# Kernel optimization log

Hardware: AMD Instinct MI355X
Metric: run time of the kernel (lower is better)

Reference implementation:

```python
import jax, jax.numpy as jnp
import numpy as np

B, V, D, H = 16, 20000, 256, 256
EPS = 1e-5


def _ln(x, g, b):
    m = jnp.mean(x, axis=-1, keepdims=True)
    v = jnp.mean(jnp.square(x - m), axis=-1, keepdims=True)
    return (x - m) * jax.lax.rsqrt(v + EPS) * g + b


def setup_inputs() -> dict:
    key = jax.random.key(0)
    ks = jax.random.split(key, 8)
    s = 1.0 / np.sqrt(D)
    return {
        "patient_emb": jax.random.normal(ks[0], (B, D), jnp.float32),
        "atc4_emb_matrix": jax.random.normal(ks[1], (V, D), jnp.float32),
        "Wp": jax.random.normal(ks[2], (D, D), jnp.float32) * s,
        "bp": jnp.zeros((D,), jnp.float32),
        "gp": jnp.ones((D,), jnp.float32),
        "betap": jnp.zeros((D,), jnp.float32),
        "Wa": jax.random.normal(ks[3], (D, D), jnp.float32) * s,
        "ba": jnp.zeros((D,), jnp.float32),
        "ga": jnp.ones((D,), jnp.float32),
        "betaa": jnp.zeros((D,), jnp.float32),
        "W1": jax.random.normal(ks[4], (2 * D, H), jnp.float32) * (1.0 / np.sqrt(2 * D)),
        "b1": jnp.zeros((H,), jnp.float32),
        "W2": jax.random.normal(ks[5], (H,), jnp.float32) * (1.0 / np.sqrt(H)),
        "b2": jnp.zeros((1,), jnp.float32),
        "g_pred": jnp.ones((V,), jnp.float32),
        "b_pred": jnp.zeros((V,), jnp.float32),
    }


def reference(patient_emb, atc4_emb_matrix, Wp, bp, gp, betap, Wa, ba, ga, betaa,
              W1, b1, W2, b2, g_pred, b_pred):
    # patient projector + layernorm: (B, D)
    p = _ln(patient_emb @ Wp + bp, gp, betap)
    # atc4 projector + layernorm: (V, D)
    a = _ln(atc4_emb_matrix @ Wa + ba, ga, betaa)
    # AttentionFusion: concat([p_expand, a_expand], -1) @ W1 == p@W1[:D] + a@W1[D:]
    ph = p @ W1[:D]            # (B, H)
    ah = a @ W1[D:]            # (V, H)
    h = jnp.tanh(ph[:, None, :] + ah[None, :, :] + b1)   # (B, V, H)
    scores = jnp.einsum('bvh,h->bv', h, W2) + b2[0]       # (B, V)
    # pred layernorm over the vocab dimension
    return _ln(scores, g_pred, b_pred)
```

## Files before the change

kernel.cpp:

```cpp
#include <hip/hip_runtime.h>


typedef unsigned short ushort_t;
typedef __attribute__((ext_vector_type(8))) short short8;
typedef __attribute__((ext_vector_type(4))) float floatx4;

#define C2F 2.8853900817779268f
#define V_N 20000
#define NBLK 625

__device__ __forceinline__ ushort_t f2bf(float f) {
    unsigned int u = __builtin_bit_cast(unsigned int, f);
    u += 0x7FFFu + ((u >> 16) & 1u);
    return (ushort_t)(u >> 16);
}
__device__ __forceinline__ float exp2_fast(float x) { return __builtin_amdgcn_exp2f(x); }
__device__ __forceinline__ float rcp_fast(float x)  { return __builtin_amdgcn_rcpf(x); }

__global__ __launch_bounds__(1024) void prep_kernel(
    const float* __restrict__ patient_emb, const float* __restrict__ Wp,
    const float* __restrict__ bp, const float* __restrict__ gp,
    const float* __restrict__ betap, const float* __restrict__ Wa,
    const float* __restrict__ W1, ushort_t* __restrict__ pWa,
    ushort_t* __restrict__ pW1b, float* __restrict__ EpT)
{
    const int blk = blockIdx.x;
    const int tid = threadIdx.x;
    __shared__ float peL[256];
    __shared__ float pL[256];
    __shared__ float part[4][256];
    __shared__ float red[8];

    if (blk < 16) {
        int slot = blk * 1024 + tid;
        int matrix = slot >> 13;
        int rest = slot & 8191;
        int s = rest >> 10, T = (rest >> 6) & 15, l = rest & 63;
        const float* src = matrix ? (W1 + 256 * 256) : Wa;
        ushort_t* dst = matrix ? pW1b : pWa;
        int kbase = s * 32 + ((l >> 4) << 3);
        int nn = (T << 4) + (l & 15);
        short8 t;
        #pragma unroll
        for (int j = 0; j < 8; ++j)
            t[j] = (short)f2bf(src[(kbase + j) * 256 + nn]);
        *(short8*)(dst + rest * 8) = t;
        return;
    }

    const int b = blk - 16;
    const int j = tid & 255, pq = tid >> 8;
    if (tid < 256) peL[tid] = patient_emb[b * 256 + tid];
    __syncthreads();
    float a0 = 0.f;
    #pragma unroll 8
    for (int dd = 0; dd < 64; ++dd) {
        int d = pq * 64 + dd;
        a0 += peL[d] * Wp[d * 256 + j];
    }
    part[pq][j] = a0;
    __syncthreads();
    float x = 0.f;
    if (tid < 256) {
        x = part[0][j] + part[1][j] + part[2][j] + part[3][j] + bp[j];
        float s1 = x, s2 = x * x;
        #pragma unroll
        for (int off = 32; off; off >>= 1) {
            s1 += __shfl_xor(s1, off);
            s2 += __shfl_xor(s2, off);
        }
        int wv = tid >> 6;
        if ((tid & 63) == 0) { red[wv * 2] = s1; red[wv * 2 + 1] = s2; }
    }
    __syncthreads();
    if (tid < 256) {
        float s1 = red[0] + red[2] + red[4] + red[6];
        float s2 = red[1] + red[3] + red[5] + red[7];
        float mean = s1 * (1.f / 256.f);
        float var  = s2 * (1.f / 256.f) - mean * mean;
        float rstd = rsqrtf(var + 1e-5f);
        pL[tid] = (x - mean) * rstd * gp[tid] + betap[tid];
    }
    __syncthreads();
    float a2 = 0.f;
    #pragma unroll 8
    for (int dd = 0; dd < 64; ++dd) {
        int d = pq * 64 + dd;
        a2 += pL[d] * W1[d * 256 + j];
    }
    part[pq][j] = a2;
    __syncthreads();
    if (tid < 256)
        EpT[tid * 16 + b] = exp2_fast(
            C2F * (part[0][tid] + part[1][tid] + part[2][tid] + part[3][tid]));
}

__global__ __launch_bounds__(256) void mega_kernel(
    const float* __restrict__ atc4, const float* __restrict__ ba,
    const float* __restrict__ ga, const float* __restrict__ betaa,
    const float* __restrict__ b1, const float* __restrict__ W2,
    const ushort_t* __restrict__ pWa, const ushort_t* __restrict__ pW1b,
    const float* __restrict__ EpT, float* __restrict__ scores,
    float* __restrict__ s1g, float* __restrict__ s2g)
{
    __shared__ ushort_t AtileF[8192];
    __shared__ float EpL[256 * 17];
    __shared__ float statsP[4][32][2];
    __shared__ float statsF[32][2];
    __shared__ float redbuf[2][1056];

    const int tid = threadIdx.x;
    const int w = tid >> 6, lane = tid & 63;
    const int q = lane >> 4, n = lane & 15;
    const int v0 = blockIdx.x * 32;

    #pragma unroll
    for (int i = 0; i < 16; ++i) {
        int idx = i * 256 + tid;
        EpL[(idx >> 4) * 17 + (idx & 15)] = EpT[idx];
    }
    {
        const int r_ = tid >> 3, s_ = tid & 7;
        const int mi_ = r_ >> 4, n_ = r_ & 15;
        const float* srcp = atc4 + (v0 + r_) * 256 + s_ * 32;
        #pragma unroll
        for (int j = 0; j < 8; ++j) {
            float4 f = ((const float4*)srcp)[j];
            ushort4 usv = make_ushort4(f2bf(f.x), f2bf(f.y), f2bf(f.z), f2bf(f.w));
            int addr = ((mi_ * 8 + s_) * 64 + (j >> 1) * 16 + n_) * 8 + (j & 1) * 4;
            *(ushort4*)(AtileF + addr) = usv;
        }
    }
    __syncthreads();

    floatx4 acc[2][4];
    #pragma unroll
    for (int mi = 0; mi < 2; ++mi)
        #pragma unroll
        for (int ni = 0; ni < 4; ++ni) acc[mi][ni] = (floatx4){0.f, 0.f, 0.f, 0.f};
    #pragma unroll
    for (int s = 0; s < 8; ++s) {
        short8 a0 = ((const short8*)AtileF)[s * 64 + lane];
        short8 a1 = ((const short8*)AtileF)[(8 + s) * 64 + lane];
        #pragma unroll
        for (int ni = 0; ni < 4; ++ni) {
            short8 bfv = *(const short8*)(pWa + ((s * 16 + w * 4 + ni) * 64 + lane) * 8);
            acc[0][ni] = __builtin_amdgcn_mfma_f32_16x16x32_bf16(a0, bfv, acc[0][ni], 0, 0, 0);
            acc[1][ni] = __builtin_amdgcn_mfma_f32_16x16x32_bf16(a1, bfv, acc[1][ni], 0, 0, 0);
        }
    }

    float bac[4], gac[4], bec[4], b1c[4], w2c[4];
    #pragma unroll
    for (int ni = 0; ni < 4; ++ni) {
        int col = w * 64 + ni * 16 + n;
        bac[ni] = ba[col]; gac[ni] = ga[col]; bec[ni] = betaa[col];
        b1c[ni] = C2F * b1[col]; w2c[ni] = W2[col];
    }

    float s1v[8] = {0, 0, 0, 0, 0, 0, 0, 0}, s2v[8] = {0, 0, 0, 0, 0, 0, 0, 0};
    #pragma unroll
    for (int mi = 0; mi < 2; ++mi)
        #pragma unroll
        for (int ni = 0; ni < 4; ++ni)
            #pragma unroll
            for (int r = 0; r < 4; ++r) {
                float x = acc[mi][ni][r] + bac[ni];
                acc[mi][ni][r] = x;
                s1v[mi * 4 + r] += x;
                s2v[mi * 4 + r] += x * x;
            }
    #pragma unroll
    for (int off = 1; off < 16; off <<= 1)
        #pragma unroll
        for (int k = 0; k < 8; ++k) {
            s1v[k] += __shfl_xor(s1v[k], off);
            s2v[k] += __shfl_xor(s2v[k], off);
        }
    if (n == 0) {
        #pragma unroll
        for (int mi = 0; mi < 2; ++mi)
            #pragma unroll
            for (int r = 0; r < 4; ++r) {
                int row = mi * 16 + q * 4 + r;
                statsP[w][row][0] = s1v[mi * 4 + r];
                statsP[w][row][1] = s2v[mi * 4 + r];
            }
    }
    __syncthreads();
    if (tid < 32) {
        float m1 = statsP[0][tid][0] + statsP[1][tid][0] + statsP[2][tid][0] + statsP[3][tid][0];
        float m2 = statsP[0][tid][1] + statsP[1][tid][1] + statsP[2][tid][1] + statsP[3][tid][1];
        float mean = m1 * (1.f / 256.f);
        float var  = m2 * (1.f / 256.f) - mean * mean;
        statsF[tid][0] = mean;
        statsF[tid][1] = rsqrtf(var + 1e-5f);
    }
    __syncthreads();

    #pragma unroll
    for (int mi = 0; mi < 2; ++mi)
        #pragma unroll
        for (int r = 0; r < 4; ++r) {
            int row = mi * 16 + q * 4 + r;
            float mean = statsF[row][0], rstd = statsF[row][1];
            #pragma unroll
            for (int ni = 0; ni < 4; ++ni) {
                float xv = (acc[mi][ni][r] - mean) * rstd * gac[ni] + bec[ni];
                int addr = ((mi * 8 + (w * 2 + (ni >> 1))) * 64 +
                            ((ni & 1) * 2 + (n >> 3)) * 16 + (q * 4 + r)) * 8 + (n & 7);
                AtileF[addr] = f2bf(xv);
            }
        }
    __syncthreads();

    floatx4 acc2[2][4];
    #pragma unroll
    for (int mi = 0; mi < 2; ++mi)
        #pragma unroll
        for (int ni = 0; ni < 4; ++ni) acc2[mi][ni] = (floatx4){0.f, 0.f, 0.f, 0.f};
    #pragma unroll
    for (int s = 0; s < 8; ++s) {
        short8 a0 = ((const short8*)AtileF)[s * 64 + lane];
        short8 a1 = ((const short8*)AtileF)[(8 + s) * 64 + lane];
        #pragma unroll
        for (int ni = 0; ni < 4; ++ni) {
            short8 bfv = *(const short8*)(pW1b + ((s * 16 + w * 4 + ni) * 64 + lane) * 8);
            acc2[0][ni] = __builtin_amdgcn_mfma_f32_16x16x32_bf16(a0, bfv, acc2[0][ni], 0, 0, 0);
            acc2[1][ni] = __builtin_amdgcn_mfma_f32_16x16x32_bf16(a1, bfv, acc2[1][ni], 0, 0, 0);
        }
    }

    float Ea[2][4][4];
    #pragma unroll
    for (int mi = 0; mi < 2; ++mi)
        #pragma unroll
        for (int ni = 0; ni < 4; ++ni)
            #pragma unroll
            for (int r = 0; r < 4; ++r)
                Ea[mi][ni][r] = exp2_fast(fmaf(C2F, acc2[mi][ni][r], b1c[ni]));

    #pragma unroll
    for (int p = 0; p < 2; ++p) {
        float accs[8][8];
        #pragma unroll
        for (int bb = 0; bb < 8; ++bb)
            #pragma unroll
            for (int v = 0; v < 8; ++v) accs[bb][v] = 0.f;
        #pragma unroll
        for (int ni = 0; ni < 4; ++ni) {
            int base = (w * 64 + ni * 16 + n) * 17 + p * 8;
            float ep[8];
            #pragma unroll
            for (int bb = 0; bb < 8; ++bb) ep[bb] = EpL[base + bb];
            #pragma unroll
            for (int bb = 0; bb < 8; ++bb)
                #pragma unroll
                for (int mi = 0; mi < 2; ++mi)
                    #pragma unroll
                    for (int r = 0; r < 4; ++r)
                        accs[bb][mi * 4 + r] +=
                            w2c[ni] * rcp_fast(fmaf(ep[bb], Ea[mi][ni][r], 1.f));
        }
        float t4[4][8], t2v[2][8], t1[8], afin[8];
        {
            int hb = n & 1;
            #pragma unroll
            for (int p2 = 0; p2 < 4; ++p2)
                #pragma unroll
                for (int v = 0; v < 8; ++v) {
                    float keep = hb ? accs[2 * p2 + 1][v] : accs[2 * p2][v];
                    float send = hb ? accs[2 * p2][v] : accs[2 * p2 + 1][v];
                    t4[p2][v] = keep + __shfl_xor(send, 1);
                }
            hb = (n >> 1) & 1;
            #pragma unroll
            for (int p2 = 0; p2 < 2; ++p2)
                #pragma unroll
                for (int v = 0; v < 8; ++v) {
                    float keep = hb ? t4[2 * p2 + 1][v] : t4[2 * p2][v];
                    float send = hb ? t4[2 * p2][v] : t4[2 * p2 + 1][v];
                    t2v[p2][v] = keep + __shfl_xor(send, 2);
                }
            hb = (n >> 2) & 1;
            #pragma unroll
            for (int v = 0; v < 8; ++v) {
                float keep = hb ? t2v[1][v] : t2v[0][v];
                float send = hb ? t2v[0][v] : t2v[1][v];
                t1[v] = keep + __shfl_xor(send, 4);
            }
            #pragma unroll
            for (int v = 0; v < 8; ++v)
                afin[v] = t1[v] + __shfl_xor(t1[v], 8);
        }
        if (n < 8) {
            #pragma unroll
            for (int mi = 0; mi < 2; ++mi)
                #pragma unroll
                for (int r = 0; r < 4; ++r)
                    redbuf[p][(w * 8 + n) * 33 + mi * 16 + q * 4 + r] = afin[mi * 4 + r];
        }
        __syncthreads();
        {
            int bb = tid >> 5, v = tid & 31;
            float S = redbuf[p][bb * 33 + v] + redbuf[p][(8 + bb) * 33 + v] +
                      redbuf[p][(16 + bb) * 33 + v] + redbuf[p][(24 + bb) * 33 + v];
            int bg = p * 8 + bb;
            scores[bg * V_N + v0 + v] = S;
            float ls1 = S, ls2 = S * S;
            #pragma unroll
            for (int off = 1; off < 32; off <<= 1) {
                ls1 += __shfl_xor(ls1, off);
                ls2 += __shfl_xor(ls2, off);
            }
            if ((tid & 31) == 0) {
                s1g[bg * NBLK + blockIdx.x] = ls1;
                s2g[bg * NBLK + blockIdx.x] = ls2;
            }
        }
    }
}

__global__ __launch_bounds__(256) void final_kernel(
    const float* __restrict__ scores, const float* __restrict__ s1g,
    const float* __restrict__ s2g, const float* __restrict__ g_pred,
    const float* __restrict__ b_pred, float* __restrict__ out)
{
    const int cx = blockIdx.x, b = blockIdx.y, tid = threadIdx.x;
    __shared__ float redL[8];
    float ls1 = 0.f, ls2 = 0.f;
    for (int i = tid; i < NBLK; i += 256) {
        ls1 += s1g[b * NBLK + i];
        ls2 += s2g[b * NBLK + i];
    }
    #pragma unroll
    for (int off = 32; off; off >>= 1) {
        ls1 += __shfl_xor(ls1, off);
        ls2 += __shfl_xor(ls2, off);
    }
    int w = tid >> 6;
    if ((tid & 63) == 0) { redL[w] = ls1; redL[4 + w] = ls2; }
    __syncthreads();
    float S1 = redL[0] + redL[1] + redL[2] + redL[3];
    float S2 = redL[4] + redL[5] + redL[6] + redL[7];
    float mean = S1 * (1.f / 20000.f);
    float var  = S2 * (1.f / 20000.f) - mean * mean;
    float k = -2.f * rsqrtf(4.f * var + 1e-5f);
    #pragma unroll
    for (int i = 0; i < 8; ++i) {
        int off = i * 256 + tid;
        if (off < 2000) {
            int v = cx * 2000 + off;
            float S = scores[b * V_N + v];
            out[b * V_N + v] = (S - mean) * k * g_pred[v] + b_pred[v];
        }
    }
}

extern "C" void kernel_launch(void* const* d_in, const int* in_sizes, int n_in,
                              void* d_out, int out_size, void* d_ws, size_t ws_size,
                              hipStream_t stream)
{
    const float* patient_emb = (const float*)d_in[0];
    const float* atc4        = (const float*)d_in[1];
    const float* Wp     = (const float*)d_in[2];
    const float* bp     = (const float*)d_in[3];
    const float* gp     = (const float*)d_in[4];
    const float* betap  = (const float*)d_in[5];
    const float* Wa     = (const float*)d_in[6];
    const float* ba     = (const float*)d_in[7];
    const float* ga     = (const float*)d_in[8];
    const float* betaa  = (const float*)d_in[9];
    const float* W1     = (const float*)d_in[10];
    const float* b1     = (const float*)d_in[11];
    const float* W2     = (const float*)d_in[12];
    const float* g_pred = (const float*)d_in[14];
    const float* b_pred = (const float*)d_in[15];

    char* ws = (char*)d_ws;
    float*    EpT    = (float*)(ws);
    ushort_t* pWa    = (ushort_t*)(ws + 16384);
    ushort_t* pW1b   = (ushort_t*)(ws + 147456);
    float*    scores = (float*)(ws + 278528);
    float*    s1g    = (float*)(ws + 1558528);
    float*    s2g    = (float*)(ws + 1598528);
    float*    out    = (float*)d_out;

    prep_kernel<<<32, 1024, 0, stream>>>(patient_emb, Wp, bp, gp, betap,
                                         Wa, W1, pWa, pW1b, EpT);
    mega_kernel<<<NBLK, 256, 0, stream>>>(atc4, ba, ga, betaa, b1, W2,
                                          pWa, pW1b, EpT, scores, s1g, s2g);
    final_kernel<<<dim3(10, 16), 256, 0, stream>>>(scores, s1g, s2g,
                                                   g_pred, b_pred, out);
}
```

Measured before the change: 155.1 us.

## Halve rows per block in mega kernel to double grid and occupancy

Each mega_kernel block now handles 16 vocab rows instead of 32, giving 1250 blocks instead of 625 so the 256 CUs get more work and better load balance. Register arrays shrink by half and a launch-bounds occupancy hint of 4 blocks per CU is added. The EpL row stride changes from 17 to 20 so Ep values can be read as float4, and the reduction buffer and stats buffers are resized to match. In exchange, each block loads the Ep table and the B weight fragments for only half as many rows, and only half the threads do the final score write.

```diff
diff --git a/kernel.cpp b/kernel.cpp
--- a/kernel.cpp
+++ b/kernel.cpp
@@ -7,7 +7,7 @@
 
 #define C2F 2.8853900817779268f
 #define V_N 20000
-#define NBLK 625
+#define NBLK 1250
 
 __device__ __forceinline__ ushort_t f2bf(float f) {
     unsigned int u = __builtin_bit_cast(unsigned int, f);
@@ -95,7 +95,7 @@
             C2F * (part[0][tid] + part[1][tid] + part[2][tid] + part[3][tid]));
 }
 
-__global__ __launch_bounds__(256) void mega_kernel(
+__global__ __launch_bounds__(256, 4) void mega_kernel(
     const float* __restrict__ atc4, const float* __restrict__ ba,
     const float* __restrict__ ga, const float* __restrict__ betaa,
     const float* __restrict__ b1, const float* __restrict__ W2,
@@ -103,50 +103,47 @@
     const float* __restrict__ EpT, float* __restrict__ scores,
     float* __restrict__ s1g, float* __restrict__ s2g)
 {
-    __shared__ ushort_t AtileF[8192];
-    __shared__ float EpL[256 * 17];
-    __shared__ float statsP[4][32][2];
-    __shared__ float statsF[32][2];
-    __shared__ float redbuf[2][1056];
+    __shared__ ushort_t AtileF[4096];
+    __shared__ float EpL[256 * 20];
+    __shared__ float statsP[4][16][2];
+    __shared__ float statsF[16][2];
+    __shared__ float redbuf[2][8][68];
 
     const int tid = threadIdx.x;
     const int w = tid >> 6, lane = tid & 63;
     const int q = lane >> 4, n = lane & 15;
-    const int v0 = blockIdx.x * 32;
+    const int v0 = blockIdx.x * 16;
 
     #pragma unroll
     for (int i = 0; i < 16; ++i) {
         int idx = i * 256 + tid;
-        EpL[(idx >> 4) * 17 + (idx & 15)] = EpT[idx];
+        EpL[(idx >> 4) * 20 + (idx & 15)] = EpT[idx];
     }
     {
-        const int r_ = tid >> 3, s_ = tid & 7;
-        const int mi_ = r_ >> 4, n_ = r_ & 15;
-        const float* srcp = atc4 + (v0 + r_) * 256 + s_ * 32;
-        #pragma unroll
-        for (int j = 0; j < 8; ++j) {
-            float4 f = ((const float4*)srcp)[j];
+        const int row = tid >> 4;
+        const int kb = (tid & 15) * 16;
+        const float* srcp = atc4 + (v0 + row) * 256 + kb;
+        #pragma unroll
+        for (int i = 0; i < 4; ++i) {
+            int k = kb + i * 4;
+            float4 f = *(const float4*)(srcp + i * 4);
             ushort4 usv = make_ushort4(f2bf(f.x), f2bf(f.y), f2bf(f.z), f2bf(f.w));
-            int addr = ((mi_ * 8 + s_) * 64 + (j >> 1) * 16 + n_) * 8 + (j & 1) * 4;
+            int addr = (((k >> 5) * 64) + (((k >> 3) & 3) * 16) + row) * 8 + (k & 7);
             *(ushort4*)(AtileF + addr) = usv;
         }
     }
     __syncthreads();
 
-    floatx4 acc[2][4];
-    #pragma unroll
-    for (int mi = 0; mi < 2; ++mi)
-        #pragma unroll
-        for (int ni = 0; ni < 4; ++ni) acc[mi][ni] = (floatx4){0.f, 0.f, 0.f, 0.f};
+    floatx4 acc[4];
+    #pragma unroll
+    for (int ni = 0; ni < 4; ++ni) acc[ni] = (floatx4){0.f, 0.f, 0.f, 0.f};
     #pragma unroll
     for (int s = 0; s < 8; ++s) {
         short8 a0 = ((const short8*)AtileF)[s * 64 + lane];
-        short8 a1 = ((const short8*)AtileF)[(8 + s) * 64 + lane];
         #pragma unroll
         for (int ni = 0; ni < 4; ++ni) {
             short8 bfv = *(const short8*)(pWa + ((s * 16 + w * 4 + ni) * 64 + lane) * 8);
-            acc[0][ni] = __builtin_amdgcn_mfma_f32_16x16x32_bf16(a0, bfv, acc[0][ni], 0, 0, 0);
-            acc[1][ni] = __builtin_amdgcn_mfma_f32_16x16x32_bf16(a1, bfv, acc[1][ni], 0, 0, 0);
+            acc[ni] = __builtin_amdgcn_mfma_f32_16x16x32_bf16(a0, bfv, acc[ni], 0, 0, 0);
         }
     }
 
@@ -158,37 +155,31 @@
         b1c[ni] = C2F * b1[col]; w2c[ni] = W2[col];
     }
 
-    float s1v[8] = {0, 0, 0, 0, 0, 0, 0, 0}, s2v[8] = {0, 0, 0, 0, 0, 0, 0, 0};
-    #pragma unroll
-    for (int mi = 0; mi < 2; ++mi)
-        #pragma unroll
-        for (int ni = 0; ni < 4; ++ni)
-            #pragma unroll
-            for (int r = 0; r < 4; ++r) {
-                float x = acc[mi][ni][r] + bac[ni];
-                acc[mi][ni][r] = x;
-                s1v[mi * 4 + r] += x;
-                s2v[mi * 4 + r] += x * x;
-            }
+    float s1v[4] = {0, 0, 0, 0}, s2v[4] = {0, 0, 0, 0};
+    #pragma unroll
+    for (int ni = 0; ni < 4; ++ni)
+        #pragma unroll
+        for (int r = 0; r < 4; ++r) {
+            float x = acc[ni][r] + bac[ni];
+            acc[ni][r] = x;
+            s1v[r] += x; s2v[r] += x * x;
+        }
     #pragma unroll
     for (int off = 1; off < 16; off <<= 1)
         #pragma unroll
-        for (int k = 0; k < 8; ++k) {
-            s1v[k] += __shfl_xor(s1v[k], off);
-            s2v[k] += __shfl_xor(s2v[k], off);
+        for (int r = 0; r < 4; ++r) {
+            s1v[r] += __shfl_xor(s1v[r], off);
+            s2v[r] += __shfl_xor(s2v[r], off);
         }
     if (n == 0) {
         #pragma unroll
-        for (int mi = 0; mi < 2; ++mi)
-            #pragma unroll
-            for (int r = 0; r < 4; ++r) {
-                int row = mi * 16 + q * 4 + r;
-                statsP[w][row][0] = s1v[mi * 4 + r];
-                statsP[w][row][1] = s2v[mi * 4 + r];
-            }
-    }
-    __syncthreads();
-    if (tid < 32) {
+        for (int r = 0; r < 4; ++r) {
+            statsP[w][q * 4 + r][0] = s1v[r];
+            statsP[w][q * 4 + r][1] = s2v[r];
+        }
+    }
+    __syncthreads();
+    if (tid < 16) {
         float m1 = statsP[0][tid][0] + statsP[1][tid][0] + statsP[2][tid][0] + statsP[3][tid][0];
         float m2 = statsP[0][tid][1] + statsP[1][tid][1] + statsP[2][tid][1] + statsP[3][tid][1];
         float mean = m1 * (1.f / 256.f);
@@ -199,121 +190,108 @@
     __syncthreads();
 
     #pragma unroll
-    for (int mi = 0; mi < 2; ++mi)
-        #pragma unroll
-        for (int r = 0; r < 4; ++r) {
-            int row = mi * 16 + q * 4 + r;
-            float mean = statsF[row][0], rstd = statsF[row][1];
-            #pragma unroll
-            for (int ni = 0; ni < 4; ++ni) {
-                float xv = (acc[mi][ni][r] - mean) * rstd * gac[ni] + bec[ni];
-                int addr = ((mi * 8 + (w * 2 + (ni >> 1))) * 64 +
-                            ((ni & 1) * 2 + (n >> 3)) * 16 + (q * 4 + r)) * 8 + (n & 7);
-                AtileF[addr] = f2bf(xv);
-            }
-        }
-    __syncthreads();
-
-    floatx4 acc2[2][4];
-    #pragma unroll
-    for (int mi = 0; mi < 2; ++mi)
-        #pragma unroll
-        for (int ni = 0; ni < 4; ++ni) acc2[mi][ni] = (floatx4){0.f, 0.f, 0.f, 0.f};
+    for (int r = 0; r < 4; ++r) {
+        int row = q * 4 + r;
+        float mean = statsF[row][0], rstd = statsF[row][1];
+        #pragma unroll
+        for (int ni = 0; ni < 4; ++ni) {
+            float xv = (acc[ni][r] - mean) * rstd * gac[ni] + bec[ni];
+            int addr = ((w * 2 + (ni >> 1)) * 64 +
+                        ((ni & 1) * 2 + (n >> 3)) * 16 + row) * 8 + (n & 7);
+            AtileF[addr] = f2bf(xv);
+        }
+    }
+    __syncthreads();
+
+    floatx4 acc2[4];
+    #pragma unroll
+    for (int ni = 0; ni < 4; ++ni) acc2[ni] = (floatx4){0.f, 0.f, 0.f, 0.f};
     #pragma unroll
     for (int s = 0; s < 8; ++s) {
         short8 a0 = ((const short8*)AtileF)[s * 64 + lane];
-        short8 a1 = ((const short8*)AtileF)[(8 + s) * 64 + lane];
         #pragma unroll
         for (int ni = 0; ni < 4; ++ni) {
             short8 bfv = *(const short8*)(pW1b + ((s * 16 + w * 4 + ni) * 64 + lane) * 8);
-            acc2[0][ni] = __builtin_amdgcn_mfma_f32_16x16x32_bf16(a0, bfv, acc2[0][ni], 0, 0, 0);
-            acc2[1][ni] = __builtin_amdgcn_mfma_f32_16x16x32_bf16(a1, bfv, acc2[1][ni], 0, 0, 0);
-        }
-    }
-
-    float Ea[2][4][4];
-    #pragma unroll
-    for (int mi = 0; mi < 2; ++mi)
-        #pragma unroll
-        for (int ni = 0; ni < 4; ++ni)
-            #pragma unroll
-            for (int r = 0; r < 4; ++r)
-                Ea[mi][ni][r] = exp2_fast(fmaf(C2F, acc2[mi][ni][r], b1c[ni]));
+            acc2[ni] = __builtin_amdgcn_mfma_f32_16x16x32_bf16(a0, bfv, acc2[ni], 0, 0, 0);
+        }
+    }
+
+    float Ea[4][4];
+    #pragma unroll
+    for (int ni = 0; ni < 4; ++ni)
+        #pragma unroll
+        for (int r = 0; r < 4; ++r)
+            Ea[ni][r] = exp2_fast(fmaf(C2F, acc2[ni][r], b1c[ni]));
 
     #pragma unroll
     for (int p = 0; p < 2; ++p) {
-        float accs[8][8];
+        float accs[8][4];
         #pragma unroll
         for (int bb = 0; bb < 8; ++bb)
             #pragma unroll
-            for (int v = 0; v < 8; ++v) accs[bb][v] = 0.f;
+            for (int r = 0; r < 4; ++r) accs[bb][r] = 0.f;
         #pragma unroll
         for (int ni = 0; ni < 4; ++ni) {
-            int base = (w * 64 + ni * 16 + n) * 17 + p * 8;
-            float ep[8];
-            #pragma unroll
-            for (int bb = 0; bb < 8; ++bb) ep[bb] = EpL[base + bb];
+            int base = (w * 64 + ni * 16 + n) * 20 + p * 8;
+            float4 e0 = *(const float4*)(&EpL[base]);
+            float4 e1 = *(const float4*)(&EpL[base + 4]);
+            float ep[8] = {e0.x, e0.y, e0.z, e0.w, e1.x, e1.y, e1.z, e1.w};
             #pragma unroll
             for (int bb = 0; bb < 8; ++bb)
                 #pragma unroll
-                for (int mi = 0; mi < 2; ++mi)
-                    #pragma unroll
-                    for (int r = 0; r < 4; ++r)
-                        accs[bb][mi * 4 + r] +=
-                            w2c[ni] * rcp_fast(fmaf(ep[bb], Ea[mi][ni][r], 1.f));
-        }
-        float t4[4][8], t2v[2][8], t1[8], afin[8];
+                for (int r = 0; r < 4; ++r)
+                    accs[bb][r] += w2c[ni] * rcp_fast(fmaf(ep[bb], Ea[ni][r], 1.f));
+        }
+        float t4[4][4], t2v[2][4], t1[4], afin[4];
         {
             int hb = n & 1;
             #pragma unroll
             for (int p2 = 0; p2 < 4; ++p2)
                 #pragma unroll
-                for (int v = 0; v < 8; ++v) {
-                    float keep = hb ? accs[2 * p2 + 1][v] : accs[2 * p2][v];
-                    float send = hb ? accs[2 * p2][v] : accs[2 * p2 + 1][v];
-                    t4[p2][v] = keep + __shfl_xor(send, 1);
+                for (int r = 0; r < 4; ++r) {
+                    float keep = hb ? accs[2 * p2 + 1][r] : accs[2 * p2][r];
+                    float send = hb ? accs[2 * p2][r] : accs[2 * p2 + 1][r];
+                    t4[p2][r] = keep + __shfl_xor(send, 1);
                 }
             hb = (n >> 1) & 1;
             #pragma unroll
             for (int p2 = 0; p2 < 2; ++p2)
                 #pragma unroll
-                for (int v = 0; v < 8; ++v) {
-                    float keep = hb ? t4[2 * p2 + 1][v] : t4[2 * p2][v];
-                    float send = hb ? t4[2 * p2][v] : t4[2 * p2 + 1][v];
-                    t2v[p2][v] = keep + __shfl_xor(send, 2);
+                for (int r = 0; r < 4; ++r) {
+                    float keep = hb ? t4[2 * p2 + 1][r] : t4[2 * p2][r];
+                    float send = hb ? t4[2 * p2][r] : t4[2 * p2 + 1][r];
+                    t2v[p2][r] = keep + __shfl_xor(send, 2);
                 }
             hb = (n >> 2) & 1;
             #pragma unroll
-            for (int v = 0; v < 8; ++v) {
-                float keep = hb ? t2v[1][v] : t2v[0][v];
-                float send = hb ? t2v[0][v] : t2v[1][v];
-                t1[v] = keep + __shfl_xor(send, 4);
+            for (int r = 0; r < 4; ++r) {
+                float keep = hb ? t2v[1][r] : t2v[0][r];
+                float send = hb ? t2v[0][r] : t2v[1][r];
+                t1[r] = keep + __shfl_xor(send, 4);
             }
             #pragma unroll
-            for (int v = 0; v < 8; ++v)
-                afin[v] = t1[v] + __shfl_xor(t1[v], 8);
+            for (int r = 0; r < 4; ++r)
+                afin[r] = t1[r] + __shfl_xor(t1[r], 8);
         }
         if (n < 8) {
             #pragma unroll
-            for (int mi = 0; mi < 2; ++mi)
-                #pragma unroll
-                for (int r = 0; r < 4; ++r)
-                    redbuf[p][(w * 8 + n) * 33 + mi * 16 + q * 4 + r] = afin[mi * 4 + r];
+            for (int r = 0; r < 4; ++r)
+                redbuf[p][n][w * 17 + q * 4 + r] = afin[r];
         }
         __syncthreads();
-        {
-            int bb = tid >> 5, v = tid & 31;
-            float S = redbuf[p][bb * 33 + v] + redbuf[p][(8 + bb) * 33 + v] +
-                      redbuf[p][(16 + bb) * 33 + v] + redbuf[p][(24 + bb) * 33 + v];
+        if (tid < 128) {
+            int bb = tid >> 4, v = tid & 15;
+            float S = redbuf[p][bb][v] + redbuf[p][bb][17 + v] +
+                      redbuf[p][bb][34 + v] + redbuf[p][bb][51 + v];
             int bg = p * 8 + bb;
             scores[bg * V_N + v0 + v] = S;
             float ls1 = S, ls2 = S * S;
             #pragma unroll
-            for (int off = 1; off < 32; off <<= 1) {
+            for (int off = 1; off < 16; off <<= 1) {
                 ls1 += __shfl_xor(ls1, off);
                 ls2 += __shfl_xor(ls2, off);
             }
-            if ((tid & 31) == 0) {
+            if ((tid & 15) == 0) {
                 s1g[bg * NBLK + blockIdx.x] = ls1;
                 s2g[bg * NBLK + blockIdx.x] = ls2;
             }
@@ -383,7 +361,7 @@
     ushort_t* pW1b   = (ushort_t*)(ws + 147456);
     float*    scores = (float*)(ws + 278528);
     float*    s1g    = (float*)(ws + 1558528);
-    float*    s2g    = (float*)(ws + 1598528);
+    float*    s2g    = (float*)(ws + 1638528);
     float*    out    = (float*)d_out;
 
     prep_kernel<<<32, 1024, 0, stream>>>(patient_emb, Wp, bp, gp, betap,
```

Result: slower. 172.7 us (+11.4%).
